# Performance work log

Hardware: AMD Instinct MI355X
Metric: run time of the kernel (lower is better)

## Reference

```python
import jax, jax.numpy as jnp
import numpy as np

NUM_EMBEDDINGS = 8192
EMBEDDING_DIM = 256
COMMITMENT_COST = 0.25
TOP_K = 3


def setup_inputs() -> dict:
    key = jax.random.key(0)
    k1, k2 = jax.random.split(key)
    inputs = jax.random.normal(k1, (16, 1024, EMBEDDING_DIM), dtype=jnp.float32)
    embedding_weight = jax.random.normal(k2, (NUM_EMBEDDINGS, EMBEDDING_DIM), dtype=jnp.float32)
    return {"inputs": inputs, "embedding_weight": embedding_weight}


def reference(inputs, embedding_weight):
    B, T, C = inputs.shape
    K = embedding_weight.shape[0]
    flat = inputs.reshape(-1, C)                      # (N, C)
    N = flat.shape[0]

    distances = (jnp.sum(flat * flat, axis=1, keepdims=True)
                 + jnp.sum(embedding_weight * embedding_weight, axis=1)
                 - 2.0 * flat @ embedding_weight.T)

    # smallest-k distances == largest-k of negated distances
    _, encoding_indices = jax.lax.top_k(-distances, TOP_K)   # (N, top_k)

    quantized = embedding_weight[encoding_indices]           # (N, top_k, C)
    quantized = quantized.reshape(B, T, TOP_K, C)
    inputs_rep = jnp.broadcast_to(inputs[:, :, None, :], quantized.shape)

    # commitment loss (eval path: no EMA buffer updates)
    e_latent_loss = jnp.mean((jax.lax.stop_gradient(quantized) - inputs_rep) ** 2)
    loss = COMMITMENT_COST * e_latent_loss

    # straight-through estimator
    quantized_st = inputs_rep + jax.lax.stop_gradient(quantized - inputs_rep)

    # avg_probs = mean over rows of the multi-hot encodings; equals histogram / N
    counts = jnp.zeros((K,), dtype=jnp.float32).at[encoding_indices.reshape(-1)].add(1.0)
    avg_probs = counts / N
    perplexity = jnp.exp(-jnp.sum(avg_probs * jnp.log(avg_probs + 1e-10)))

    return loss, quantized_st, perplexity, encoding_indices, distances
```

## Files before the change

### kernel.cpp

```cpp
#include <hip/hip_runtime.h>
#include <stdint.h>

#define N_ROWS 16384
#define N_EMB  8192
#define C_DIM  256
#define NKT    8

#define OFF_LOSS 0ull
#define OFF_Q    1ull
#define OFF_PERP 12582913ull
#define OFF_IDX  12582914ull
#define OFF_DIST 12632066ull

typedef short bf16x8 __attribute__((ext_vector_type(8)));
typedef float f32x4  __attribute__((ext_vector_type(4)));
typedef float f32x2  __attribute__((ext_vector_type(2)));

__device__ __forceinline__ unsigned short f2bf_rne(float f){
  unsigned u = __float_as_uint(f);
  unsigned r = 0x7fffu + ((u >> 16) & 1u);
  return (unsigned short)((u + r) >> 16);
}

__global__ __launch_bounds__(256) void k_prep(
    const float* __restrict__ X, const float* __restrict__ E,
    short* __restrict__ XT, short* __restrict__ ET,
    float* __restrict__ xnorm, float* __restrict__ enorm)
{
  int b = blockIdx.x; int tid = threadIdx.x;
  const float* src; short* dst; float* nrm; int r0, NR;
  if (b < N_ROWS / 8){ r0 = b * 8;                src = X; dst = XT; nrm = xnorm; NR = N_ROWS; }
  else               { r0 = (b - N_ROWS / 8) * 8; src = E; dst = ET; nrm = enorm; NR = N_EMB;  }
  int e = tid & 7, rsub = (tid >> 3) & 7, qg = tid >> 6;
  int row = r0 + rsub;
  float s = 0.f;
  #pragma unroll
  for (int qq = 0; qq < 8; qq++){
    int q = qg * 8 + qq;
    float x = src[(size_t)row * C_DIM + q * 8 + e];
    dst[((size_t)q * NR + row) * 8 + e] = (short)f2bf_rne(x);
    s += x * x;
  }
  __shared__ float red[8][33];
  red[rsub][qg * 8 + e] = s;
  __syncthreads();
  if (tid < 8){
    float t = 0.f;
    #pragma unroll
    for (int i = 0; i < 32; i++) t += red[tid][i];
    nrm[r0 + tid] = t;
  }
}

__device__ __forceinline__ void gload16(void* lds, const void* g){
  __builtin_amdgcn_global_load_lds(
      (const __attribute__((address_space(1))) void*)g,
      (__attribute__((address_space(3))) void*)lds, 16, 0, 0);
}

__global__ __launch_bounds__(512, 2) void k_gemm(
    const short* __restrict__ XT, const short* __restrict__ ET,
    const float* __restrict__ xnorm, const float* __restrict__ enorm,
    float* __restrict__ out)
{
  __shared__ __align__(16) short As[2][4 * 256 * 8];
  __shared__ __align__(16) short Bs[2][4 * 256 * 8];
  int tid = threadIdx.x;
  int lane = tid & 63, w = tid >> 6;
  int wr = w >> 2, wc = w & 3;
  int id = blockIdx.x;
  int x = id & 7, jj = id >> 3, c = jj >> 5, u = jj & 31;
  int bm = c * 8 + (u >> 2);
  int bn = x * 4 + (u & 3);

  f32x4 acc[8][4];
  #pragma unroll
  for (int m = 0; m < 8; m++)
    #pragma unroll
    for (int n = 0; n < 4; n++) acc[m][n] = (f32x4){0.f, 0.f, 0.f, 0.f};

  auto stage = [&](int buf, int kt){
    #pragma unroll
    for (int i = 0; i < 4; i++){
      int p = w * 4 + i;
      if (p < 16){
        int q = p >> 2, qr = p & 3;
        gload16(&As[buf][(q * 256 + qr * 64) * 8],
                XT + ((size_t)(kt * 4 + q) * N_ROWS + (size_t)bm * 256 + qr * 64 + lane) * 8);
      } else {
        int pb = p - 16; int q = pb >> 2, qr = pb & 3;
        gload16(&Bs[buf][(q * 256 + qr * 64) * 8],
                ET + ((size_t)(kt * 4 + q) * N_EMB + (size_t)bn * 256 + qr * 64 + lane) * 8);
      }
    }
  };

  int r15 = lane & 15, lg4 = lane >> 4;

  stage(0, 0); stage(1, 1);

  #pragma unroll
  for (int t = 0; t < NKT; ++t){
    const int buf = t & 1;
    if (t < NKT - 1) { asm volatile("s_waitcnt vmcnt(4)" ::: "memory"); }
    else             { asm volatile("s_waitcnt vmcnt(0)" ::: "memory"); }
    __builtin_amdgcn_s_barrier();

    bf16x8 af[8], bf[4];
    {
      int q = lg4;
      #pragma unroll
      for (int m = 0; m < 8; m++)
        af[m] = *(const bf16x8*)&As[buf][(q * 256 + wr * 128 + m * 16 + r15) * 8];
      #pragma unroll
      for (int n = 0; n < 4; n++)
        bf[n] = *(const bf16x8*)&Bs[buf][(q * 256 + wc * 64 + n * 16 + r15) * 8];
    }
    __builtin_amdgcn_s_setprio(1);
    #pragma unroll
    for (int m = 0; m < 4; m++)
      #pragma unroll
      for (int n = 0; n < 4; n++)
        acc[m][n] = __builtin_amdgcn_mfma_f32_16x16x32_bf16(af[m], bf[n], acc[m][n], 0, 0, 0);
    __builtin_amdgcn_s_setprio(0);

    asm volatile("s_waitcnt lgkmcnt(0)" ::: "memory");
    __builtin_amdgcn_sched_barrier(0);
    __builtin_amdgcn_s_barrier();
    if (t < NKT - 2) stage(buf, t + 2);

    __builtin_amdgcn_s_setprio(1);
    #pragma unroll
    for (int m = 4; m < 8; m++)
      #pragma unroll
      for (int n = 0; n < 4; n++)
        acc[m][n] = __builtin_amdgcn_mfma_f32_16x16x32_bf16(af[m], bf[n], acc[m][n], 0, 0, 0);
    __builtin_amdgcn_s_setprio(0);
  }

  int lc = lane & 15;
  #pragma unroll
  for (int m = 0; m < 8; m++){
    int rb = bm * 256 + wr * 128 + m * 16 + lg4 * 4;
    float xn0 = xnorm[rb], xn1 = xnorm[rb+1], xn2 = xnorm[rb+2], xn3 = xnorm[rb+3];
    #pragma unroll
    for (int n = 0; n < 4; n++){
      int col = bn * 256 + wc * 64 + n * 16 + lc;
      float en = enorm[col];
      out[OFF_DIST + (size_t)(rb + 0) * N_EMB + col] = xn0 + en - 2.0f * acc[m][n][0];
      out[OFF_DIST + (size_t)(rb + 1) * N_EMB + col] = xn1 + en - 2.0f * acc[m][n][1];
      out[OFF_DIST + (size_t)(rb + 2) * N_EMB + col] = xn2 + en - 2.0f * acc[m][n][2];
      out[OFF_DIST + (size_t)(rb + 3) * N_EMB + col] = xn3 + en - 2.0f * acc[m][n][3];
    }
  }
}

#define LT(av,ai,bv,bi) (((av) < (bv)) || ((av) == (bv) && (ai) < (bi)))

__global__ __launch_bounds__(256) void k_tq(
    const float* __restrict__ X, const float* __restrict__ E,
    float* out, int* __restrict__ counts, float* __restrict__ partials)
{
  int row = blockIdx.x; int tid = threadIdx.x;
  const f32x4* drow = (const f32x4*)(out + OFF_DIST + (size_t)row * N_EMB);
  float v0 = __builtin_inff(), v1 = __builtin_inff(), v2 = __builtin_inff();
  int   i0 = 0x7fffffff,       i1 = 0x7fffffff,       i2 = 0x7fffffff;
  for (int i = tid; i < N_EMB / 4; i += 256){
    f32x4 dv = __builtin_nontemporal_load(&drow[i]);
    #pragma unroll
    for (int j = 0; j < 4; j++){
      float d = dv[j]; int ii = i * 4 + j;
      if (LT(d, ii, v2, i2)){
        if (LT(d, ii, v1, i1)){
          v2 = v1; i2 = i1;
          if (LT(d, ii, v0, i0)){ v1 = v0; i1 = i0; v0 = d; i0 = ii; }
          else                  { v1 = d;  i1 = ii; }
        } else { v2 = d; i2 = ii; }
      }
    }
  }
  #pragma unroll
  for (int off = 1; off < 64; off <<= 1){
    float b0 = __shfl_xor(v0, off), b1 = __shfl_xor(v1, off), b2 = __shfl_xor(v2, off);
    int   j0 = __shfl_xor(i0, off), j1 = __shfl_xor(i1, off), j2 = __shfl_xor(i2, off);
    float a0 = v0, a1 = v1, a2 = v2; int x0 = i0, x1 = i1, x2 = i2;
    float r0, r1, r2; int s0, s1, s2;
    if (LT(a0, x0, b0, j0)){ r0 = a0; s0 = x0; a0 = a1; x0 = x1; a1 = a2; x1 = x2; a2 = __builtin_inff(); x2 = 0x7fffffff; }
    else                   { r0 = b0; s0 = j0; b0 = b1; j0 = j1; b1 = b2; j1 = j2; b2 = __builtin_inff(); j2 = 0x7fffffff; }
    if (LT(a0, x0, b0, j0)){ r1 = a0; s1 = x0; a0 = a1; x0 = x1; a1 = a2; x1 = x2; a2 = __builtin_inff(); x2 = 0x7fffffff; }
    else                   { r1 = b0; s1 = j0; b0 = b1; j0 = j1; b1 = b2; j1 = j2; b2 = __builtin_inff(); j2 = 0x7fffffff; }
    if (LT(a0, x0, b0, j0)){ r2 = a0; s2 = x0; }
    else                   { r2 = b0; s2 = j0; }
    v0 = r0; i0 = s0; v1 = r1; i1 = s1; v2 = r2; i2 = s2;
  }
  __shared__ float swv[4][3]; __shared__ int swi[4][3];
  int lane = tid & 63, wid = tid >> 6;
  if (lane == 0){
    swv[wid][0] = v0; swv[wid][1] = v1; swv[wid][2] = v2;
    swi[wid][0] = i0; swi[wid][1] = i1; swi[wid][2] = i2;
  }
  __syncthreads();
  if (tid == 0){
    for (int wq = 1; wq < 4; wq++){
      for (int t = 0; t < 3; t++){
        float d = swv[wq][t]; int i = swi[wq][t];
        if (LT(d, i, v2, i2)){
          if (LT(d, i, v1, i1)){
            v2 = v1; i2 = i1;
            if (LT(d, i, v0, i0)){ v1 = v0; i1 = i0; v0 = d; i0 = i; }
            else                 { v1 = d;  i1 = i; }
          } else { v2 = d; i2 = i; }
        }
      }
    }
    out[OFF_IDX + (size_t)row * 3 + 0] = (float)i0;
    out[OFF_IDX + (size_t)row * 3 + 1] = (float)i1;
    out[OFF_IDX + (size_t)row * 3 + 2] = (float)i2;
    swi[0][0] = i0; swi[0][1] = i1; swi[0][2] = i2;
    atomicAdd(&counts[i0], 1); atomicAdd(&counts[i1], 1); atomicAdd(&counts[i2], 1);
  }
  __syncthreads();
  int fi0 = swi[0][0], fi1 = swi[0][1], fi2 = swi[0][2];
  float xv = X[(size_t)row * C_DIM + tid];
  float lsum = 0.f;
  {
    float e = E[(size_t)fi0 * C_DIM + tid]; float d = e - xv;
    out[OFF_Q + ((size_t)row * 3 + 0) * C_DIM + tid] = xv + d; lsum += d * d;
  }
  {
    float e = E[(size_t)fi1 * C_DIM + tid]; float d = e - xv;
    out[OFF_Q + ((size_t)row * 3 + 1) * C_DIM + tid] = xv + d; lsum += d * d;
  }
  {
    float e = E[(size_t)fi2 * C_DIM + tid]; float d = e - xv;
    out[OFF_Q + ((size_t)row * 3 + 2) * C_DIM + tid] = xv + d; lsum += d * d;
  }
  __shared__ float qred[256];
  qred[tid] = lsum; __syncthreads();
  for (int s = 128; s > 0; s >>= 1){ if (tid < s) qred[tid] += qred[tid + s]; __syncthreads(); }
  if (tid == 0) partials[row] = qred[0];
}

__global__ __launch_bounds__(256) void k_final(
    const float* __restrict__ partials, const int* __restrict__ counts,
    float* __restrict__ out)
{
  int t = threadIdx.x;
  float ls = 0.f;
  for (int i = t; i < N_ROWS; i += 256) ls += partials[i];
  float es = 0.f;
  for (int i = t; i < N_EMB; i += 256){
    float p = (float)counts[i] * (1.0f / 16384.0f);
    es += p * logf(p + 1e-10f);
  }
  __shared__ float r1[256], r2[256];
  r1[t] = ls; r2[t] = es; __syncthreads();
  for (int s = 128; s > 0; s >>= 1){
    if (t < s){ r1[t] += r1[t + s]; r2[t] += r2[t + s]; }
    __syncthreads();
  }
  if (t == 0){
    out[OFF_LOSS] = 0.25f * r1[0] / 12582912.0f;
    out[OFF_PERP] = expf(-r2[0]);
  }
}

extern "C" void kernel_launch(void* const* d_in, const int* in_sizes, int n_in,
                              void* d_out, int out_size, void* d_ws, size_t ws_size,
                              hipStream_t stream)
{
  const float* X = (const float*)d_in[0];
  const float* E = (const float*)d_in[1];
  float* out = (float*)d_out;
  char* ws = (char*)d_ws;
  short* XT       = (short*)(ws + 0);
  short* ET       = (short*)(ws + 8388608);
  float* xnorm    = (float*)(ws + 12582912);
  float* enorm    = (float*)(ws + 12648448);
  int*   counts   = (int*)  (ws + 12681216);
  float* partials = (float*)(ws + 12713984);

  hipMemsetAsync(counts, 0, N_EMB * sizeof(int), stream);
  k_prep<<<(N_ROWS + N_EMB) / 8, 256, 0, stream>>>(X, E, XT, ET, xnorm, enorm);
  k_gemm<<<2048, 512, 0, stream>>>(XT, ET, xnorm, enorm, out);
  k_tq<<<N_ROWS, 256, 0, stream>>>(X, E, out, counts, partials);
  k_final<<<1, 256, 0, stream>>>(partials, counts, out);
}
```

Baseline: 347.0 us.

## Recompute top-3 via MFMA instead of rereading the distance matrix

Replaces the top-k kernel that streamed the full 16384x8192 distance matrix back from global memory. A new kernel recomputes the dot products with bf16 MFMA from the prepped transposed inputs, keeps a per-lane top-3 in registers, and writes 24 partial candidates per row. A second kernel merges those candidates one wavefront per row and does the gather, loss and counts with vectorized loads. This saves the 512MB reread at the cost of running the GEMM a second time, and drops the xnorm term from the selection (it is constant per row, so ranking is unchanged).

```diff
diff --git a/kernel.cpp b/kernel.cpp
--- a/kernel.cpp
+++ b/kernel.cpp
@@ -15,6 +15,34 @@
 typedef short bf16x8 __attribute__((ext_vector_type(8)));
 typedef float f32x4  __attribute__((ext_vector_type(4)));
 typedef float f32x2  __attribute__((ext_vector_type(2)));
+
+#define LT(av,ai,bv,bi) (((av) < (bv)) || ((av) == (bv) && (ai) < (bi)))
+
+__device__ __forceinline__ void ins3(float d, int ii,
+    float& v0, int& i0, float& v1, int& i1, float& v2, int& i2){
+  if (LT(d, ii, v2, i2)){
+    if (LT(d, ii, v1, i1)){
+      v2 = v1; i2 = i1;
+      if (LT(d, ii, v0, i0)){ v1 = v0; i1 = i0; v0 = d; i0 = ii; }
+      else                  { v1 = d;  i1 = ii; }
+    } else { v2 = d; i2 = ii; }
+  }
+}
+
+__device__ __forceinline__ void mrg3(int off,
+    float& v0, int& i0, float& v1, int& i1, float& v2, int& i2){
+  float b0 = __shfl_xor(v0, off), b1 = __shfl_xor(v1, off), b2 = __shfl_xor(v2, off);
+  int   j0 = __shfl_xor(i0, off), j1 = __shfl_xor(i1, off), j2 = __shfl_xor(i2, off);
+  float a0 = v0, a1 = v1, a2 = v2; int x0 = i0, x1 = i1, x2 = i2;
+  float r0, r1, r2; int s0, s1, s2;
+  if (LT(a0, x0, b0, j0)){ r0 = a0; s0 = x0; a0 = a1; x0 = x1; a1 = a2; x1 = x2; a2 = __builtin_inff(); x2 = 0x7fffffff; }
+  else                   { r0 = b0; s0 = j0; b0 = b1; j0 = j1; b1 = b2; j1 = j2; b2 = __builtin_inff(); j2 = 0x7fffffff; }
+  if (LT(a0, x0, b0, j0)){ r1 = a0; s1 = x0; a0 = a1; x0 = x1; a1 = a2; x1 = x2; a2 = __builtin_inff(); x2 = 0x7fffffff; }
+  else                   { r1 = b0; s1 = j0; b0 = b1; j0 = j1; b1 = b2; j1 = j2; b2 = __builtin_inff(); j2 = 0x7fffffff; }
+  if (LT(a0, x0, b0, j0)){ r2 = a0; s2 = x0; }
+  else                   { r2 = b0; s2 = j0; }
+  v0 = r0; i0 = s0; v1 = r1; i1 = s1; v2 = r2; i2 = s2;
+}
 
 __device__ __forceinline__ unsigned short f2bf_rne(float f){
   unsigned u = __float_as_uint(f);
@@ -155,90 +183,107 @@
   }
 }
 
-#define LT(av,ai,bv,bi) (((av) < (bv)) || ((av) == (bv) && (ai) < (bi)))
-
-__global__ __launch_bounds__(256) void k_tq(
-    const float* __restrict__ X, const float* __restrict__ E,
+__global__ __launch_bounds__(256) void k_t3(
+    const short* __restrict__ XT, const short* __restrict__ ET,
+    const float* __restrict__ enorm, f32x2* __restrict__ partial)
+{
+  int tid = threadIdx.x; int lane = tid & 63, w = tid >> 6;
+  int b = blockIdx.x;
+  int xg = b >> 1, h = b & 1;
+  int r15 = lane & 15, lg4 = lane >> 4;
+  int xbase = xg * 64;
+
+  bf16x8 xf[4][8];
+  #pragma unroll
+  for (int xs = 0; xs < 4; xs++)
+    #pragma unroll
+    for (int ks = 0; ks < 8; ks++)
+      xf[xs][ks] = *(const bf16x8*)&XT[((size_t)(ks * 4 + lg4) * N_ROWS + xbase + xs * 16 + r15) * 8];
+
+  float tv0[4], tv1[4], tv2[4]; int ti0[4], ti1[4], ti2[4];
+  #pragma unroll
+  for (int xs = 0; xs < 4; xs++){
+    tv0[xs] = tv1[xs] = tv2[xs] = __builtin_inff();
+    ti0[xs] = ti1[xs] = ti2[xs] = 0x7fffffff;
+  }
+
+  int eb0 = h * 4096 + w * 1024;
+  for (int et = 0; et < 64; et++){
+    int eb = eb0 + et * 16;
+    f32x4 acc[4];
+    #pragma unroll
+    for (int xs = 0; xs < 4; xs++) acc[xs] = (f32x4){0.f, 0.f, 0.f, 0.f};
+    #pragma unroll
+    for (int ks = 0; ks < 8; ks++){
+      bf16x8 ef = *(const bf16x8*)&ET[((size_t)(ks * 4 + lg4) * N_EMB + eb + r15) * 8];
+      #pragma unroll
+      for (int xs = 0; xs < 4; xs++)
+        acc[xs] = __builtin_amdgcn_mfma_f32_16x16x32_bf16(ef, xf[xs][ks], acc[xs], 0, 0, 0);
+    }
+    #pragma unroll
+    for (int j = 0; j < 4; j++){
+      int er = eb + lg4 * 4 + j;
+      float en = enorm[er];
+      #pragma unroll
+      for (int xs = 0; xs < 4; xs++){
+        float d = en - 2.0f * acc[xs][j];
+        ins3(d, er, tv0[xs], ti0[xs], tv1[xs], ti1[xs], tv2[xs], ti2[xs]);
+      }
+    }
+  }
+  #pragma unroll
+  for (int xs = 0; xs < 4; xs++){
+    mrg3(16, tv0[xs], ti0[xs], tv1[xs], ti1[xs], tv2[xs], ti2[xs]);
+    mrg3(32, tv0[xs], ti0[xs], tv1[xs], ti1[xs], tv2[xs], ti2[xs]);
+  }
+  if (lane < 16){
+    #pragma unroll
+    for (int xs = 0; xs < 4; xs++){
+      int row = xbase + xs * 16 + lane;
+      size_t base = ((size_t)row * 8 + h * 4 + w) * 3;
+      partial[base + 0] = (f32x2){tv0[xs], __int_as_float(ti0[xs])};
+      partial[base + 1] = (f32x2){tv1[xs], __int_as_float(ti1[xs])};
+      partial[base + 2] = (f32x2){tv2[xs], __int_as_float(ti2[xs])};
+    }
+  }
+}
+
+__global__ __launch_bounds__(256) void k_mq(
+    const f32x2* __restrict__ partial, const float* __restrict__ X, const float* __restrict__ E,
     float* out, int* __restrict__ counts, float* __restrict__ partials)
 {
-  int row = blockIdx.x; int tid = threadIdx.x;
-  const f32x4* drow = (const f32x4*)(out + OFF_DIST + (size_t)row * N_EMB);
+  int wid = threadIdx.x >> 6, lane = threadIdx.x & 63;
+  int row = blockIdx.x * 4 + wid;
+  const f32x2* pr = partial + (size_t)row * 24;
   float v0 = __builtin_inff(), v1 = __builtin_inff(), v2 = __builtin_inff();
   int   i0 = 0x7fffffff,       i1 = 0x7fffffff,       i2 = 0x7fffffff;
-  for (int i = tid; i < N_EMB / 4; i += 256){
-    f32x4 dv = __builtin_nontemporal_load(&drow[i]);
-    #pragma unroll
-    for (int j = 0; j < 4; j++){
-      float d = dv[j]; int ii = i * 4 + j;
-      if (LT(d, ii, v2, i2)){
-        if (LT(d, ii, v1, i1)){
-          v2 = v1; i2 = i1;
-          if (LT(d, ii, v0, i0)){ v1 = v0; i1 = i0; v0 = d; i0 = ii; }
-          else                  { v1 = d;  i1 = ii; }
-        } else { v2 = d; i2 = ii; }
-      }
-    }
-  }
-  #pragma unroll
-  for (int off = 1; off < 64; off <<= 1){
-    float b0 = __shfl_xor(v0, off), b1 = __shfl_xor(v1, off), b2 = __shfl_xor(v2, off);
-    int   j0 = __shfl_xor(i0, off), j1 = __shfl_xor(i1, off), j2 = __shfl_xor(i2, off);
-    float a0 = v0, a1 = v1, a2 = v2; int x0 = i0, x1 = i1, x2 = i2;
-    float r0, r1, r2; int s0, s1, s2;
-    if (LT(a0, x0, b0, j0)){ r0 = a0; s0 = x0; a0 = a1; x0 = x1; a1 = a2; x1 = x2; a2 = __builtin_inff(); x2 = 0x7fffffff; }
-    else                   { r0 = b0; s0 = j0; b0 = b1; j0 = j1; b1 = b2; j1 = j2; b2 = __builtin_inff(); j2 = 0x7fffffff; }
-    if (LT(a0, x0, b0, j0)){ r1 = a0; s1 = x0; a0 = a1; x0 = x1; a1 = a2; x1 = x2; a2 = __builtin_inff(); x2 = 0x7fffffff; }
-    else                   { r1 = b0; s1 = j0; b0 = b1; j0 = j1; b1 = b2; j1 = j2; b2 = __builtin_inff(); j2 = 0x7fffffff; }
-    if (LT(a0, x0, b0, j0)){ r2 = a0; s2 = x0; }
-    else                   { r2 = b0; s2 = j0; }
-    v0 = r0; i0 = s0; v1 = r1; i1 = s1; v2 = r2; i2 = s2;
-  }
-  __shared__ float swv[4][3]; __shared__ int swi[4][3];
-  int lane = tid & 63, wid = tid >> 6;
+  if (lane < 24){ f32x2 p = pr[lane]; ins3(p[0], __float_as_int(p[1]), v0, i0, v1, i1, v2, i2); }
+  #pragma unroll
+  for (int off = 1; off < 64; off <<= 1)
+    mrg3(off, v0, i0, v1, i1, v2, i2);
   if (lane == 0){
-    swv[wid][0] = v0; swv[wid][1] = v1; swv[wid][2] = v2;
-    swi[wid][0] = i0; swi[wid][1] = i1; swi[wid][2] = i2;
-  }
-  __syncthreads();
-  if (tid == 0){
-    for (int wq = 1; wq < 4; wq++){
-      for (int t = 0; t < 3; t++){
-        float d = swv[wq][t]; int i = swi[wq][t];
-        if (LT(d, i, v2, i2)){
-          if (LT(d, i, v1, i1)){
-            v2 = v1; i2 = i1;
-            if (LT(d, i, v0, i0)){ v1 = v0; i1 = i0; v0 = d; i0 = i; }
-            else                 { v1 = d;  i1 = i; }
-          } else { v2 = d; i2 = i; }
-        }
-      }
-    }
     out[OFF_IDX + (size_t)row * 3 + 0] = (float)i0;
     out[OFF_IDX + (size_t)row * 3 + 1] = (float)i1;
     out[OFF_IDX + (size_t)row * 3 + 2] = (float)i2;
-    swi[0][0] = i0; swi[0][1] = i1; swi[0][2] = i2;
     atomicAdd(&counts[i0], 1); atomicAdd(&counts[i1], 1); atomicAdd(&counts[i2], 1);
   }
-  __syncthreads();
-  int fi0 = swi[0][0], fi1 = swi[0][1], fi2 = swi[0][2];
-  float xv = X[(size_t)row * C_DIM + tid];
+  int c4 = lane * 4;
+  f32x4 x4 = *(const f32x4*)&X[(size_t)row * C_DIM + c4];
+  int idx[3] = {i0, i1, i2};
   float lsum = 0.f;
-  {
-    float e = E[(size_t)fi0 * C_DIM + tid]; float d = e - xv;
-    out[OFF_Q + ((size_t)row * 3 + 0) * C_DIM + tid] = xv + d; lsum += d * d;
-  }
-  {
-    float e = E[(size_t)fi1 * C_DIM + tid]; float d = e - xv;
-    out[OFF_Q + ((size_t)row * 3 + 1) * C_DIM + tid] = xv + d; lsum += d * d;
-  }
-  {
-    float e = E[(size_t)fi2 * C_DIM + tid]; float d = e - xv;
-    out[OFF_Q + ((size_t)row * 3 + 2) * C_DIM + tid] = xv + d; lsum += d * d;
-  }
-  __shared__ float qred[256];
-  qred[tid] = lsum; __syncthreads();
-  for (int s = 128; s > 0; s >>= 1){ if (tid < s) qred[tid] += qred[tid + s]; __syncthreads(); }
-  if (tid == 0) partials[row] = qred[0];
+  #pragma unroll
+  for (int t = 0; t < 3; t++){
+    f32x4 e4 = *(const f32x4*)&E[(size_t)idx[t] * C_DIM + c4];
+    #pragma unroll
+    for (int q = 0; q < 4; q++){
+      float diff = e4[q] - x4[q];
+      out[OFF_Q + ((size_t)row * 3 + t) * C_DIM + c4 + q] = x4[q] + diff;
+      lsum += diff * diff;
+    }
+  }
+  #pragma unroll
+  for (int off = 32; off > 0; off >>= 1) lsum += __shfl_down(lsum, off);
+  if (lane == 0) partials[row] = lsum;
 }
 
 __global__ __launch_bounds__(256) void k_final(
@@ -277,12 +322,14 @@
   short* ET       = (short*)(ws + 8388608);
   float* xnorm    = (float*)(ws + 12582912);
   float* enorm    = (float*)(ws + 12648448);
-  int*   counts   = (int*)  (ws + 12681216);
-  float* partials = (float*)(ws + 12713984);
+  f32x2* partial  = (f32x2*)(ws + 12681216);
+  int*   counts   = (int*)  (ws + 15826944);
+  float* partials = (float*)(ws + 15859712);
 
   hipMemsetAsync(counts, 0, N_EMB * sizeof(int), stream);
   k_prep<<<(N_ROWS + N_EMB) / 8, 256, 0, stream>>>(X, E, XT, ET, xnorm, enorm);
   k_gemm<<<2048, 512, 0, stream>>>(XT, ET, xnorm, enorm, out);
-  k_tq<<<N_ROWS, 256, 0, stream>>>(X, E, out, counts, partials);
+  k_t3<<<512, 256, 0, stream>>>(XT, ET, enorm, partial);
+  k_mq<<<N_ROWS / 4, 256, 0, stream>>>(partial, X, E, out, counts, partials);
   k_final<<<1, 256, 0, stream>>>(partials, counts, out);
 }
```

Measured after the change: 770.5 us. 2.22x slower.
